# Optimization experiments

Measured on AMD Instinct MI355X. Metric: run time of the kernel, lower is better.

## Reference

```python
import jax, jax.numpy as jnp
import numpy as np

EPS = 1e-5


def _bn_linear(x, g, b, W, c, relu):
    # BatchNorm1d over flattened (B*N) axis with batch statistics (training mode),
    # then Linear, then optional ReLU. x: [B, N, Din]
    mean = jnp.mean(x, axis=(0, 1))
    var = jnp.mean(jnp.square(x - mean), axis=(0, 1))  # biased variance, as torch BN uses in fwd
    xn = (x - mean) * jax.lax.rsqrt(var + EPS) * g + b
    y = jnp.einsum('bnd,od->bno', xn, W) + c
    return jax.nn.relu(y) if relu else y


def setup_inputs() -> dict:
    key = jax.random.key(0)
    ks = jax.random.split(key, 8)
    B, N = 32, 2048
    dims = [256, 512, 512, 1024]  # in_size, hidden_sizes..., out_size
    inp = {"set_feats": jax.random.normal(ks[0], (B, N, dims[0]), dtype=jnp.float32)}
    for i, (din, dout) in enumerate(zip(dims[:-1], dims[1:])):
        inp[f"g{i}"] = jnp.ones((din,), jnp.float32)
        inp[f"b{i}"] = jnp.zeros((din,), jnp.float32)
        inp[f"W{i}"] = jax.random.normal(ks[1 + i], (dout, din), dtype=jnp.float32) / np.sqrt(din)
        inp[f"c{i}"] = jax.random.normal(ks[4 + i], (dout,), dtype=jnp.float32) * 0.01
    return inp


def reference(set_feats, g0, b0, W0, c0, g1, b1, W1, c1, g2, b2, W2, c2):
    x = _bn_linear(set_feats, g0, b0, W0, c0, relu=True)
    x = _bn_linear(x, g1, b1, W1, c1, relu=True)
    x = _bn_linear(x, g2, b2, W2, c2, relu=False)
    # reduction = 'max' over the set dimension (-2)
    return jnp.max(x, axis=-2)
```

## Files before the change

### kernel.cpp

```cpp
#include <hip/hip_runtime.h>
#include <hip/hip_bf16.h>
#include <stdint.h>

typedef unsigned short u16;
typedef __attribute__((ext_vector_type(8))) __bf16 bf16x8;
typedef __attribute__((ext_vector_type(4))) float f32x4;

#define BN_EPS 1e-5f
#define MROWS 65536
#define INV_M (1.0f / 65536.0f)
#define NREP 16

__device__ __forceinline__ u16 f2bf(float f) {
  unsigned u = __builtin_bit_cast(unsigned, f);
  unsigned r = (u + 0x7FFFu + ((u >> 16) & 1u)) >> 16;
  return (u16)r;
}
__device__ __forceinline__ float bf2f(u16 h) {
  return __builtin_bit_cast(float, (unsigned)h << 16);
}

__global__ __launch_bounds__(256)
void stats_cast_k(const float* __restrict__ x, u16* __restrict__ xbf,
                  float* __restrict__ srep ) {
  const int t = threadIdx.x;
  const int tc = t & 63, tr = t >> 6;
  const int rb = blockIdx.x * 32 + tr * 8;
  float4 v[8];
#pragma unroll
  for (int i = 0; i < 8; ++i)
    v[i] = *(const float4*)(x + (size_t)(rb + i) * 256 + tc * 4);
  float s0 = 0, s1 = 0, s2 = 0, s3 = 0, q0 = 0, q1 = 0, q2 = 0, q3 = 0;
#pragma unroll
  for (int i = 0; i < 8; ++i) {
    ushort4 ov;
    ov.x = f2bf(v[i].x); ov.y = f2bf(v[i].y);
    ov.z = f2bf(v[i].z); ov.w = f2bf(v[i].w);
    *(ushort4*)(xbf + (size_t)(rb + i) * 256 + tc * 4) = ov;
    s0 += v[i].x; q0 += v[i].x * v[i].x;
    s1 += v[i].y; q1 += v[i].y * v[i].y;
    s2 += v[i].z; q2 += v[i].z * v[i].z;
    s3 += v[i].w; q3 += v[i].w * v[i].w;
  }
  __shared__ float red[4][256];
  red[tr][tc * 4 + 0] = s0; red[tr][tc * 4 + 1] = s1;
  red[tr][tc * 4 + 2] = s2; red[tr][tc * 4 + 3] = s3;
  __syncthreads();
  float* dst = srep + (blockIdx.x & (NREP - 1)) * 512;
  if (tr == 0) {
#pragma unroll
    for (int i = 0; i < 4; ++i) {
      int c = tc * 4 + i;
      atomicAdd(&dst[c], red[0][c] + red[1][c] + red[2][c] + red[3][c]);
    }
  }
  __syncthreads();
  red[tr][tc * 4 + 0] = q0; red[tr][tc * 4 + 1] = q1;
  red[tr][tc * 4 + 2] = q2; red[tr][tc * 4 + 3] = q3;
  __syncthreads();
  if (tr == 0) {
#pragma unroll
    for (int i = 0; i < 4; ++i) {
      int c = tc * 4 + i;
      atomicAdd(&dst[256 + c], red[0][c] + red[1][c] + red[2][c] + red[3][c]);
    }
  }
}

__global__ __launch_bounds__(256)
void prep_w_k(const float* __restrict__ W, const float* __restrict__ g,
              const float* __restrict__ b, const float* __restrict__ c,
              const float* __restrict__ ssum, const float* __restrict__ ssq,
              int rep_stride, int nrep,
              u16* __restrict__ Wp, float* __restrict__ cp, int din, int dout) {
  const int gw = (blockIdx.x * 256 + threadIdx.x) >> 6;
  const int l = threadIdx.x & 63;
  if (gw >= dout) return;
  const int o = gw;
  float acc = 0.f;
  for (int d0 = l * 4; d0 < din; d0 += 256) {
    float sm[4] = {}, sq[4] = {};
    for (int r = 0; r < nrep; ++r) {
      float4 a = *(const float4*)(ssum + (size_t)r * rep_stride + d0);
      float4 z = *(const float4*)(ssq + (size_t)r * rep_stride + d0);
      sm[0] += a.x; sm[1] += a.y; sm[2] += a.z; sm[3] += a.w;
      sq[0] += z.x; sq[1] += z.y; sq[2] += z.z; sq[3] += z.w;
    }
    float4 wv = *(const float4*)(W + (size_t)o * din + d0);
    float4 gv = *(const float4*)(g + d0);
    float4 bv = *(const float4*)(b + d0);
    float w4[4] = {wv.x, wv.y, wv.z, wv.w};
    float g4[4] = {gv.x, gv.y, gv.z, gv.w};
    float b4[4] = {bv.x, bv.y, bv.z, bv.w};
    ushort4 ov;
    u16 o4[4];
#pragma unroll
    for (int i = 0; i < 4; ++i) {
      float mean = sm[i] * INV_M;
      float var = sq[i] * INV_M - mean * mean;
      float alpha = g4[i] * rsqrtf(var + BN_EPS);
      float beta = b4[i] - mean * alpha;
      o4[i] = f2bf(w4[i] * alpha);
      acc += w4[i] * beta;
    }
    ov.x = o4[0]; ov.y = o4[1]; ov.z = o4[2]; ov.w = o4[3];
    *(ushort4*)(Wp + (size_t)o * din + d0) = ov;
  }
#pragma unroll
  for (int off = 32; off > 0; off >>= 1) acc += __shfl_xor(acc, off, 64);
  if (l == 0) cp[o] = c[o] + acc;
}

#define GLDS16(gp, lp) __builtin_amdgcn_global_load_lds( \
    (__attribute__((address_space(1))) void*)(void*)(gp), \
    (__attribute__((address_space(3))) void*)(lp), 16, 0, 0)

template <int KDIM, int NDIM, bool RELU, bool DOMAX>
__device__ __forceinline__
void gemm_body(const u16* __restrict__ A, const u16* __restrict__ B,
               const float* __restrict__ cp, u16* __restrict__ Y,
               float* __restrict__ osum, float* __restrict__ osq,
               unsigned* __restrict__ maxbuf) {
  constexpr int NK = KDIM >> 5;
  __shared__ __align__(16) u16 lds[8 * 8192];
  const int t = threadIdx.x;
  const int w = t >> 6, l = t & 63;
  const int lr = l & 15, lk = l >> 4;
  const int wm = w >> 2, wn = w & 3;

  const int cpx = (int)gridDim.x >> 3;
  int bid = (int)blockIdx.x;
  bid = (bid & 7) * cpx + (bid >> 3);
  constexpr int TILES_N = NDIM >> 8;
  const int tm0 = (bid / TILES_N) << 8;
  const int tn0 = (bid % TILES_N) << 8;

  const int srow = t >> 2;
  const int scol = (((t & 3) ^ ((t >> 3) & 3)) << 3);
  const u16* Ag = A + (size_t)(tm0 + srow) * KDIM + scol;
  const u16* Bg = B + (size_t)(tn0 + srow) * KDIM + scol;
  u16* const ldsA = lds;
  u16* const ldsB = lds + 4 * 8192;

#define STAGE_A(slot_, kt_) do { \
    GLDS16(Ag + (kt_) * 32, ldsA + (slot_) * 8192 + t * 8); \
    GLDS16(Ag + (size_t)128 * KDIM + (kt_) * 32, ldsA + (slot_) * 8192 + 4096 + t * 8); \
  } while (0)
#define STAGE_B(slot_, kt_) do { \
    GLDS16(Bg + (kt_) * 32, ldsB + (slot_) * 8192 + t * 8); \
    GLDS16(Bg + (size_t)128 * KDIM + (kt_) * 32, ldsB + (slot_) * 8192 + 4096 + t * 8); \
  } while (0)

  const int pc = (lk ^ ((lr >> 1) & 3)) * 8;
  const int rba = wm * 128 + lr;
  const int rbb = wn * 64 + lr;

  f32x4 acc[8][4] = {};

  STAGE_A(0, 0); STAGE_B(0, 0);
  STAGE_A(1, 1); STAGE_B(1, 1);
  STAGE_A(2, 2); STAGE_B(2, 2);
  asm volatile("s_waitcnt vmcnt(8)" ::: "memory");
  __builtin_amdgcn_s_barrier();

#pragma unroll
  for (int T = 0; T < NK; ++T) {
    const int sl = T & 3;
    const u16* la = ldsA + sl * 8192;
    const u16* lb = ldsB + sl * 8192;
    bf16x8 af[4], bf[4];
#pragma unroll
    for (int n = 0; n < 4; ++n)
      bf[n] = *(const bf16x8*)(lb + (rbb + n * 16) * 32 + pc);
#pragma unroll
    for (int j = 0; j < 4; ++j)
      af[j] = *(const bf16x8*)(la + (rba + j * 16) * 32 + pc);
    if (T + 3 < NK) STAGE_A((T + 3) & 3, T + 3);
    __builtin_amdgcn_s_barrier();
    __builtin_amdgcn_s_setprio(1);
#pragma unroll
    for (int j = 0; j < 4; ++j)
#pragma unroll
      for (int n = 0; n < 4; ++n)
        acc[j][n] = __builtin_amdgcn_mfma_f32_16x16x32_bf16(af[j], bf[n], acc[j][n], 0, 0, 0);
    __builtin_amdgcn_s_setprio(0);
    __builtin_amdgcn_s_barrier();
#pragma unroll
    for (int j = 0; j < 4; ++j)
      af[j] = *(const bf16x8*)(la + (rba + 64 + j * 16) * 32 + pc);
    if (T + 3 < NK) STAGE_B((T + 3) & 3, T + 3);
    if (T < NK - 3)       asm volatile("s_waitcnt vmcnt(8)" ::: "memory");
    else if (T == NK - 3) asm volatile("s_waitcnt vmcnt(4)" ::: "memory");
    else if (T == NK - 2) asm volatile("s_waitcnt vmcnt(0)" ::: "memory");
    __builtin_amdgcn_s_barrier();
    __builtin_amdgcn_s_setprio(1);
#pragma unroll
    for (int j = 0; j < 4; ++j)
#pragma unroll
      for (int n = 0; n < 4; ++n)
        acc[4 + j][n] = __builtin_amdgcn_mfma_f32_16x16x32_bf16(af[j], bf[n], acc[4 + j][n], 0, 0, 0);
    __builtin_amdgcn_s_setprio(0);
    __builtin_amdgcn_s_barrier();
  }
#undef STAGE_A
#undef STAGE_B

  if (!DOMAX) {
    float cs[4] = {}, cq[4] = {};
#pragma unroll
    for (int n = 0; n < 4; ++n) {
      const int gcol = tn0 + wn * 64 + n * 16 + lr;
      const float cb = cp[gcol];
#pragma unroll
      for (int m = 0; m < 8; ++m) {
        const int grow = tm0 + wm * 128 + m * 16 + lk * 4;
#pragma unroll
        for (int r = 0; r < 4; ++r) {
          float v = acc[m][n][r] + cb;
          if (RELU) v = fmaxf(v, 0.f);
          Y[(size_t)(grow + r) * NDIM + gcol] = f2bf(v);
          cs[n] += v;
          cq[n] += v * v;
        }
      }
    }
    if (RELU) {
#pragma unroll
      for (int n = 0; n < 4; ++n) {
        cs[n] += __shfl_xor(cs[n], 16, 64);
        cs[n] += __shfl_xor(cs[n], 32, 64);
        cq[n] += __shfl_xor(cq[n], 16, 64);
        cq[n] += __shfl_xor(cq[n], 32, 64);
      }
      float* sred = (float*)lds;
      __syncthreads();
      if (lk == 0) {
#pragma unroll
        for (int n = 0; n < 4; ++n) {
          const int c = wn * 64 + n * 16 + lr;
          sred[wm * 256 + c] = cs[n];
          sred[512 + wm * 256 + c] = cq[n];
        }
      }
      __syncthreads();
      if (t < 256) {
        atomicAdd(&osum[tn0 + t], sred[t] + sred[256 + t]);
      } else {
        const int c = t - 256;
        atomicAdd(&osq[tn0 + c], sred[512 + c] + sred[768 + c]);
      }
    }
  } else {
    const int batch = tm0 >> 11;
#pragma unroll
    for (int n = 0; n < 4; ++n) {
      const int gcol = tn0 + wn * 64 + n * 16 + lr;
      const float cb = cp[gcol];
      float mx = -3.0e38f;
#pragma unroll
      for (int m = 0; m < 8; ++m)
#pragma unroll
        for (int r = 0; r < 4; ++r)
          mx = fmaxf(mx, acc[m][n][r] + cb);
      mx = fmaxf(mx, __shfl_xor(mx, 16, 64));
      mx = fmaxf(mx, __shfl_xor(mx, 32, 64));
      if (lk == 0) {
        unsigned u = __builtin_bit_cast(unsigned, mx);
        u = (u & 0x80000000u) ? ~u : (u | 0x80000000u);
        atomicMax(&maxbuf[batch * NDIM + gcol], u);
      }
    }
  }
}

__global__ __launch_bounds__(512, 2)
void gemm_l0(const u16* __restrict__ A, const u16* __restrict__ B,
             const float* __restrict__ cp, u16* __restrict__ Y,
             float* __restrict__ osum, float* __restrict__ osq) {
  gemm_body<256, 512, true, false>(A, B, cp, Y, osum, osq, nullptr);
}
__global__ __launch_bounds__(512, 2)
void gemm_l1(const u16* __restrict__ A, const u16* __restrict__ B,
             const float* __restrict__ cp, u16* __restrict__ Y,
             float* __restrict__ osum, float* __restrict__ osq) {
  gemm_body<512, 512, true, false>(A, B, cp, Y, osum, osq, nullptr);
}
__global__ __launch_bounds__(512, 2)
void gemm_l2(const u16* __restrict__ A, const u16* __restrict__ B,
             const float* __restrict__ cp, unsigned* __restrict__ maxbuf) {
  gemm_body<512, 1024, false, true>(A, B, cp, nullptr, nullptr, nullptr, maxbuf);
}

__global__ void decode_k(const unsigned* __restrict__ mb, float* __restrict__ out, int n) {
  int i = blockIdx.x * 256 + threadIdx.x;
  if (i < n) {
    unsigned u = mb[i];
    u = (u & 0x80000000u) ? (u & 0x7FFFFFFFu) : ~u;
    out[i] = __builtin_bit_cast(float, u);
  }
}

extern "C" void kernel_launch(void* const* d_in, const int* in_sizes, int n_in,
                              void* d_out, int out_size, void* d_ws, size_t ws_size,
                              hipStream_t stream) {
  const float* x0 = (const float*)d_in[0];
  const float* g0 = (const float*)d_in[1];
  const float* b0 = (const float*)d_in[2];
  const float* W0 = (const float*)d_in[3];
  const float* c0 = (const float*)d_in[4];
  const float* g1 = (const float*)d_in[5];
  const float* b1 = (const float*)d_in[6];
  const float* W1 = (const float*)d_in[7];
  const float* c1 = (const float*)d_in[8];
  const float* g2 = (const float*)d_in[9];
  const float* b2 = (const float*)d_in[10];
  const float* W2 = (const float*)d_in[11];
  const float* c2 = (const float*)d_in[12];

  char* ws = (char*)d_ws;
  size_t off = 0;
  auto alloc = [&](size_t bytes) -> char* {
    char* p = ws + off;
    off += (bytes + 255) & ~(size_t)255;
    return p;
  };
  u16* x0bf = (u16*)alloc((size_t)MROWS * 256 * 2);
  u16* y1 = (u16*)alloc((size_t)MROWS * 512 * 2);
  u16* y2 = (u16*)alloc((size_t)MROWS * 512 * 2);
  float* s0rep = (float*)alloc((NREP * 512 + 1024 + 1024 + 32768) * 4);
  float* s1sum = s0rep + NREP * 512;
  float* s1sq = s1sum + 512;
  float* s2sum = s1sum + 1024;
  float* s2sq = s2sum + 512;
  unsigned* maxbuf = (unsigned*)(s1sum + 2048);
  const size_t zbytes = (size_t)(NREP * 512 + 2048 + 32768) * 4;
  u16* W0p = (u16*)alloc(512 * 256 * 2);
  u16* W1p = (u16*)alloc(512 * 512 * 2);
  u16* W2p = (u16*)alloc(1024 * 512 * 2);
  float* c0p = (float*)alloc(512 * 4);
  float* c1p = (float*)alloc(512 * 4);
  float* c2p = (float*)alloc(1024 * 4);
  if (off > ws_size) return;

  hipMemsetAsync(s0rep, 0, zbytes, stream);

  stats_cast_k<<<2048, 256, 0, stream>>>(x0, x0bf, s0rep);
  prep_w_k<<<128, 256, 0, stream>>>(W0, g0, b0, c0, s0rep, s0rep + 256, 512, NREP,
                                    W0p, c0p, 256, 512);
  gemm_l0<<<512, 512, 0, stream>>>(x0bf, W0p, c0p, y1, s1sum, s1sq);
  prep_w_k<<<128, 256, 0, stream>>>(W1, g1, b1, c1, s1sum, s1sq, 0, 1,
                                    W1p, c1p, 512, 512);
  gemm_l1<<<512, 512, 0, stream>>>(y1, W1p, c1p, y2, s2sum, s2sq);
  prep_w_k<<<256, 256, 0, stream>>>(W2, g2, b2, c2, s2sum, s2sq, 0, 1,
                                    W2p, c2p, 512, 1024);
  gemm_l2<<<1024, 512, 0, stream>>>(y2, W2p, c2p, maxbuf);
  decode_k<<<128, 256, 0, stream>>>(maxbuf, (float*)d_out, 32768);
}
```

Before: 204.0 us.

## Switch GEMM inner loop to 32x32x16 MFMA tiles and drop two barriers

Replaces the 16x16x32 bf16 MFMA tiling with 32x32x16 instructions, reorganising the per-wave register tiles, the LDS read swizzle and the epilogue row/column mapping to fit. Larger MFMA tiles need fewer LDS fragment reads per FLOP and fewer instructions. The change also removes two s_barrier calls per K iteration, which cuts sync overhead but risks an LDS read/write race on the rotating stage slots if the remaining barriers do not cover it.

New measurement: 201.2 us. Within noise of the previous version (-1.4%).

```diff
diff --git a/kernel.cpp b/kernel.cpp
--- a/kernel.cpp
+++ b/kernel.cpp
@@ -4,7 +4,7 @@
 
 typedef unsigned short u16;
 typedef __attribute__((ext_vector_type(8))) __bf16 bf16x8;
-typedef __attribute__((ext_vector_type(4))) float f32x4;
+typedef __attribute__((ext_vector_type(16))) float f32x16;
 
 #define BN_EPS 1e-5f
 #define MROWS 65536
@@ -125,7 +125,7 @@
   __shared__ __align__(16) u16 lds[8 * 8192];
   const int t = threadIdx.x;
   const int w = t >> 6, l = t & 63;
-  const int lr = l & 15, lk = l >> 4;
+  const int l31 = l & 31, hi = l >> 5;
   const int wm = w >> 2, wn = w & 3;
 
   const int cpx = (int)gridDim.x >> 3;
@@ -151,11 +151,13 @@
     GLDS16(Bg + (size_t)128 * KDIM + (kt_) * 32, ldsB + (slot_) * 8192 + 4096 + t * 8); \
   } while (0)
 
-  const int pc = (lk ^ ((lr >> 1) & 3)) * 8;
-  const int rba = wm * 128 + lr;
-  const int rbb = wn * 64 + lr;
-
-  f32x4 acc[8][4] = {};
+#define RD(base_, row_, kc_) \
+  (*(const bf16x8*)((base_) + (row_) * 32 + ((((kc_) << 1) + hi) ^ (((row_) >> 1) & 3)) * 8))
+
+  const int rba = wm * 128 + l31;
+  const int rbb = wn * 64 + l31;
+
+  f32x16 acc[4][2] = {};
 
   STAGE_A(0, 0); STAGE_B(0, 0);
   STAGE_A(1, 1); STAGE_B(1, 1);
@@ -168,26 +170,33 @@
     const int sl = T & 3;
     const u16* la = ldsA + sl * 8192;
     const u16* lb = ldsB + sl * 8192;
-    bf16x8 af[4], bf[4];
-#pragma unroll
-    for (int n = 0; n < 4; ++n)
-      bf[n] = *(const bf16x8*)(lb + (rbb + n * 16) * 32 + pc);
-#pragma unroll
-    for (int j = 0; j < 4; ++j)
-      af[j] = *(const bf16x8*)(la + (rba + j * 16) * 32 + pc);
+    bf16x8 af[2][2], bf[2][2];
+#pragma unroll
+    for (int nt = 0; nt < 2; ++nt)
+#pragma unroll
+      for (int kc = 0; kc < 2; ++kc)
+        bf[nt][kc] = RD(lb, rbb + nt * 32, kc);
+#pragma unroll
+    for (int mt = 0; mt < 2; ++mt)
+#pragma unroll
+      for (int kc = 0; kc < 2; ++kc)
+        af[mt][kc] = RD(la, rba + mt * 32, kc);
     if (T + 3 < NK) STAGE_A((T + 3) & 3, T + 3);
     __builtin_amdgcn_s_barrier();
     __builtin_amdgcn_s_setprio(1);
 #pragma unroll
-    for (int j = 0; j < 4; ++j)
-#pragma unroll
-      for (int n = 0; n < 4; ++n)
-        acc[j][n] = __builtin_amdgcn_mfma_f32_16x16x32_bf16(af[j], bf[n], acc[j][n], 0, 0, 0);
+    for (int kc = 0; kc < 2; ++kc)
+#pragma unroll
+      for (int mt = 0; mt < 2; ++mt)
+#pragma unroll
+        for (int nt = 0; nt < 2; ++nt)
+          acc[mt][nt] = __builtin_amdgcn_mfma_f32_32x32x16_bf16(af[mt][kc], bf[nt][kc], acc[mt][nt], 0, 0, 0);
     __builtin_amdgcn_s_setprio(0);
-    __builtin_amdgcn_s_barrier();
-#pragma unroll
-    for (int j = 0; j < 4; ++j)
-      af[j] = *(const bf16x8*)(la + (rba + 64 + j * 16) * 32 + pc);
+#pragma unroll
+    for (int mt = 0; mt < 2; ++mt)
+#pragma unroll
+      for (int kc = 0; kc < 2; ++kc)
+        af[mt][kc] = RD(la, rba + 64 + mt * 32, kc);
     if (T + 3 < NK) STAGE_B((T + 3) & 3, T + 3);
     if (T < NK - 3)       asm volatile("s_waitcnt vmcnt(8)" ::: "memory");
     else if (T == NK - 3) asm volatile("s_waitcnt vmcnt(4)" ::: "memory");
@@ -195,51 +204,51 @@
     __builtin_amdgcn_s_barrier();
     __builtin_amdgcn_s_setprio(1);
 #pragma unroll
-    for (int j = 0; j < 4; ++j)
-#pragma unroll
-      for (int n = 0; n < 4; ++n)
-        acc[4 + j][n] = __builtin_amdgcn_mfma_f32_16x16x32_bf16(af[j], bf[n], acc[4 + j][n], 0, 0, 0);
+    for (int kc = 0; kc < 2; ++kc)
+#pragma unroll
+      for (int mt = 0; mt < 2; ++mt)
+#pragma unroll
+        for (int nt = 0; nt < 2; ++nt)
+          acc[2 + mt][nt] = __builtin_amdgcn_mfma_f32_32x32x16_bf16(af[mt][kc], bf[nt][kc], acc[2 + mt][nt], 0, 0, 0);
     __builtin_amdgcn_s_setprio(0);
-    __builtin_amdgcn_s_barrier();
   }
 #undef STAGE_A
 #undef STAGE_B
+#undef RD
 
   if (!DOMAX) {
-    float cs[4] = {}, cq[4] = {};
-#pragma unroll
-    for (int n = 0; n < 4; ++n) {
-      const int gcol = tn0 + wn * 64 + n * 16 + lr;
+    float cs[2] = {}, cq[2] = {};
+#pragma unroll
+    for (int nt = 0; nt < 2; ++nt) {
+      const int gcol = tn0 + wn * 64 + nt * 32 + l31;
       const float cb = cp[gcol];
 #pragma unroll
-      for (int m = 0; m < 8; ++m) {
-        const int grow = tm0 + wm * 128 + m * 16 + lk * 4;
-#pragma unroll
-        for (int r = 0; r < 4; ++r) {
-          float v = acc[m][n][r] + cb;
+      for (int mt = 0; mt < 4; ++mt) {
+#pragma unroll
+        for (int rg = 0; rg < 16; ++rg) {
+          const int grow = tm0 + wm * 128 + mt * 32 + (rg & 3) + 8 * (rg >> 2) + 4 * hi;
+          float v = acc[mt][nt][rg] + cb;
           if (RELU) v = fmaxf(v, 0.f);
-          Y[(size_t)(grow + r) * NDIM + gcol] = f2bf(v);
-          cs[n] += v;
-          cq[n] += v * v;
+          Y[(size_t)grow * NDIM + gcol] = f2bf(v);
+          cs[nt] += v;
+          cq[nt] += v * v;
         }
       }
     }
     if (RELU) {
 #pragma unroll
-      for (int n = 0; n < 4; ++n) {
-        cs[n] += __shfl_xor(cs[n], 16, 64);
-        cs[n] += __shfl_xor(cs[n], 32, 64);
-        cq[n] += __shfl_xor(cq[n], 16, 64);
-        cq[n] += __shfl_xor(cq[n], 32, 64);
+      for (int nt = 0; nt < 2; ++nt) {
+        cs[nt] += __shfl_xor(cs[nt], 32, 64);
+        cq[nt] += __shfl_xor(cq[nt], 32, 64);
       }
       float* sred = (float*)lds;
       __syncthreads();
-      if (lk == 0) {
-#pragma unroll
-        for (int n = 0; n < 4; ++n) {
-          const int c = wn * 64 + n * 16 + lr;
-          sred[wm * 256 + c] = cs[n];
-          sred[512 + wm * 256 + c] = cq[n];
+      if (hi == 0) {
+#pragma unroll
+        for (int nt = 0; nt < 2; ++nt) {
+          const int c = wn * 64 + nt * 32 + l31;
+          sred[wm * 256 + c] = cs[nt];
+          sred[512 + wm * 256 + c] = cq[nt];
         }
       }
       __syncthreads();
@@ -253,18 +262,17 @@
   } else {
     const int batch = tm0 >> 11;
 #pragma unroll
-    for (int n = 0; n < 4; ++n) {
-      const int gcol = tn0 + wn * 64 + n * 16 + lr;
+    for (int nt = 0; nt < 2; ++nt) {
+      const int gcol = tn0 + wn * 64 + nt * 32 + l31;
       const float cb = cp[gcol];
       float mx = -3.0e38f;
 #pragma unroll
-      for (int m = 0; m < 8; ++m)
-#pragma unroll
-        for (int r = 0; r < 4; ++r)
-          mx = fmaxf(mx, acc[m][n][r] + cb);
-      mx = fmaxf(mx, __shfl_xor(mx, 16, 64));
+      for (int mt = 0; mt < 4; ++mt)
+#pragma unroll
+        for (int rg = 0; rg < 16; ++rg)
+          mx = fmaxf(mx, acc[mt][nt][rg] + cb);
       mx = fmaxf(mx, __shfl_xor(mx, 32, 64));
-      if (lk == 0) {
+      if (hi == 0) {
         unsigned u = __builtin_bit_cast(unsigned, mx);
         u = (u & 0x80000000u) ? ~u : (u | 0x80000000u);
         atomicMax(&maxbuf[batch * NDIM + gcol], u);
```
